# Kernel tuning notes

Hardware: AMD Instinct MI355X
Metric: run time of the kernel (lower is better)

Reference implementation:

```python
import jax, jax.numpy as jnp
import numpy as np

B, S, E, H, L = 64, 256, 640, 512, 2  # batch, seq_len, input_size(=embed+sum_depth), rnn_size, num_layers
ZDIM = L * 2 * 2 * H  # ziphidden output dim = num_layers * num_dirs * (h|c) * H = 4096


def setup_inputs() -> dict:
    key = jax.random.key(0)
    ks = jax.random.split(key, 16)
    s = 0.05  # small init scale (~1/sqrt(H)) to avoid gate saturation
    f32 = jnp.float32
    inp = {
        "input": jax.random.normal(ks[0], (B, S, E), f32),
        "eps": jax.random.normal(ks[1], (B, ZDIM), f32),
        # layer 0 (input E), stacked over 2 directions [fwd, rev]
        "w_ih0": jax.random.normal(ks[2], (2, 4 * H, E), f32) * s,
        "w_hh0": jax.random.normal(ks[3], (2, 4 * H, H), f32) * s,
        "b_ih0": jax.random.normal(ks[4], (2, 4 * H), f32) * s,
        "b_hh0": jax.random.normal(ks[5], (2, 4 * H), f32) * s,
        # layer 1 (input 2H from bidirectional layer-0 output)
        "w_ih1": jax.random.normal(ks[6], (2, 4 * H, 2 * H), f32) * s,
        "w_hh1": jax.random.normal(ks[7], (2, 4 * H, H), f32) * s,
        "b_ih1": jax.random.normal(ks[8], (2, 4 * H), f32) * s,
        "b_hh1": jax.random.normal(ks[9], (2, 4 * H), f32) * s,
        # linear heads (layer_dim*2 -> layer_dim*2)
        "W_mu": jax.random.normal(ks[10], (ZDIM, ZDIM), f32) * 0.02,
        "b_mu": jax.random.normal(ks[11], (ZDIM,), f32) * 0.02,
        "W_var": jax.random.normal(ks[12], (ZDIM, ZDIM), f32) * 0.02,
        "b_var": jax.random.normal(ks[13], (ZDIM,), f32) * 0.02,
    }
    return inp


def _lstm_cell(x, h, c, wih, whh, b):
    # gates order i, f, g, o (PyTorch convention)
    g = x @ wih.T + h @ whh.T + b
    i, f, gg, o = jnp.split(g, 4, axis=-1)
    c2 = jax.nn.sigmoid(f) * c + jax.nn.sigmoid(i) * jnp.tanh(gg)
    h2 = jax.nn.sigmoid(o) * jnp.tanh(c2)
    return h2, c2


def reference(input, eps, w_ih0, w_hh0, b_ih0, b_hh0, w_ih1, w_hh1, b_ih1, b_hh1, W_mu, b_mu, W_var, b_var):
    # Module does input.view(seq_len, batch, embed) (a reshape, not transpose) then
    # steps the LSTM one timestep at a time for seq_len-1 steps. Since each call is
    # a length-1 sequence, both directions see the same single step independently.
    x_seq = input.reshape(S, B, E)[: S - 1]
    W_ih, W_hh = [w_ih0, w_ih1], [w_hh0, w_hh1]
    Bias = [b_ih0 + b_hh0, b_ih1 + b_hh1]

    h0 = jnp.zeros((2 * L, B, H), input.dtype)  # [l0f, l0r, l1f, l1r]
    c0 = jnp.zeros((2 * L, B, H), input.dtype)

    def step(carry, x):
        h, c = carry
        hs, cs = [], []
        inp_l = x
        for l in range(L):
            hf, cf = _lstm_cell(inp_l, h[2 * l], c[2 * l], W_ih[l][0], W_hh[l][0], Bias[l][0])
            hr, cr = _lstm_cell(inp_l, h[2 * l + 1], c[2 * l + 1], W_ih[l][1], W_hh[l][1], Bias[l][1])
            hs += [hf, hr]
            cs += [cf, cr]
            inp_l = jnp.concatenate([hf, hr], axis=-1)  # layer output feeds next layer
        return (jnp.stack(hs), jnp.stack(cs)), None

    (hF, cF), _ = jax.lax.scan(step, (h0, c0), x_seq)

    # ziphidden: cat(h, c, dim=2) -> transpose(0,1) -> view(B, -1)
    z = jnp.concatenate([hF, cF], axis=2)            # [2L, B, 2H]
    z = jnp.transpose(z, (1, 0, 2)).reshape(B, -1)   # [B, ZDIM]

    mu = z @ W_mu.T + b_mu
    logvar = z @ W_var.T + b_var
    # reparameterize (training mode) with externally supplied eps
    return mu + eps * jnp.exp(0.5 * logvar)
```

## Files before the change

kernel.cpp:

```cpp
#include <hip/hip_runtime.h>
#include <hip/hip_bf16.h>
#include <cstddef>
#include <cstdint>

#define B     64
#define S     256
#define E     640
#define H     512
#define TSTEPS (S - 1)
#define ZDIM  4096
#define KT    64
#define HS    (B * H)
#define CELL64 8192
#define NBUF  4

typedef __attribute__((ext_vector_type(8)))  __bf16 bf16x8;
typedef __attribute__((ext_vector_type(16))) float  f32x16;
typedef unsigned long long ull;

__device__ __forceinline__ float sigf(float x) { return 1.0f / (1.0f + __expf(-x)); }
__device__ __forceinline__ float tanhfast(float x) { return 1.0f - 2.0f / (__expf(2.0f * x) + 1.0f); }

__device__ __forceinline__ unsigned short f2bf(float f) {
    union { float f; unsigned u; } x; x.f = f;
    unsigned r = x.u + 0x7fffu + ((x.u >> 16) & 1u);
    return (unsigned short)(r >> 16);
}
__device__ __forceinline__ float bf2f(unsigned short u) {
    union { unsigned u; float f; } x; x.u = ((unsigned)u) << 16;
    return x.f;
}
__device__ __forceinline__ unsigned pk2(float a, float b) {
    return (unsigned)f2bf(a) | ((unsigned)f2bf(b) << 16);
}

#define HSTORE64(p, v) __hip_atomic_store((p), (v), __ATOMIC_RELAXED, __HIP_MEMORY_SCOPE_AGENT)
#define HSTORE32(p, v) __hip_atomic_store((p), (v), __ATOMIC_RELAXED, __HIP_MEMORY_SCOPE_AGENT)

__device__ __forceinline__ uint4 cld16(const void* p) {
    uint4 v;
    asm volatile("global_load_dwordx4 %0, %1, off sc0 sc1"
                 : "=v"(v) : "v"(p) : "memory");
    return v;
}
__device__ __forceinline__ unsigned ldf(const unsigned* p) {
    unsigned v;
    asm volatile("global_load_dword %0, %1, off sc0 sc1"
                 : "=v"(v) : "v"(p) : "memory");
    return v;
}
__device__ __forceinline__ void cwait0() {
    asm volatile("s_waitcnt vmcnt(0)" ::: "memory");
    __builtin_amdgcn_sched_barrier(0);
}
__device__ __forceinline__ bf16x8 u2b(uint4 u) {
    union { uint4 u; bf16x8 b; } x; x.u = u; return x.b;
}


__global__ __launch_bounds__(256) void conv_x_kernel(
    const float* __restrict__ in, unsigned short* __restrict__ out, int n8)
{
    int i = blockIdx.x * 256 + threadIdx.x;
    if (i >= n8) return;
    const float4* p = (const float4*)(in + (size_t)i * 8);
    float4 a = p[0], b = p[1];
    unsigned short* o = out + (size_t)i * 8;
    o[0] = f2bf(a.x); o[1] = f2bf(a.y); o[2] = f2bf(a.z); o[3] = f2bf(a.w);
    o[4] = f2bf(b.x); o[5] = f2bf(b.y); o[6] = f2bf(b.z); o[7] = f2bf(b.w);
}

__global__ __launch_bounds__(256) void repack_w_kernel(
    const float* __restrict__ in, unsigned short* __restrict__ out, int K)
{
    int kc = K / 8;
    int i = blockIdx.x * 256 + threadIdx.x;
    if (i >= 2 * 2048 * kc) return;
    int k8 = i % kc;
    int n  = (i / kc) & 2047;
    int d  = i / (kc * 2048);
    int srow = (n & 3) * 512 + (n >> 2);
    const float* src = in + ((size_t)d * 2048 + srow) * K + (size_t)k8 * 8;
    unsigned short* dst = out + ((size_t)d * 2048 + n) * K + (size_t)k8 * 8;
    #pragma unroll
    for (int q = 0; q < 8; ++q) dst[q] = f2bf(src[q]);
}

__global__ __launch_bounds__(256) void pack_bias_kernel(
    const float* __restrict__ bih, const float* __restrict__ bhh, float* __restrict__ out)
{
    int i = blockIdx.x * 256 + threadIdx.x;
    if (i >= 4096) return;
    int d = i >> 11, n = i & 2047;
    int s = d * 2048 + (n & 3) * 512 + (n >> 2);
    out[i] = bih[s] + bhh[s];
}

__global__ __launch_bounds__(256) void xproj_kernel(
    const unsigned short* __restrict__ xb,
    const unsigned short* __restrict__ w0p,
    unsigned short* __restrict__ xp)
{
    extern __shared__ __align__(16) char lds[];
    const int tid = threadIdx.x;
    const int l   = tid & 63;
    const int w   = tid >> 6;
    const int wm  = w & 1, wn = w >> 1;
    const int d   = blockIdx.x >> 5;
    const int n0  = (blockIdx.x & 31) * 64;

    for (int idx = tid; idx < 64 * 80; idx += 256) {
        int r = idx / 80, k8 = idx % 80;
        bf16x8 v = *(const bf16x8*)(w0p + ((size_t)d*2048 + n0 + r)*640 + (size_t)k8*8);
        int o = k8*16 + r*16; o -= (o >= 1280) ? 1280 : 0;
        *(bf16x8*)(lds + r*1280 + o) = v;
    }
    __syncthreads();

    const int lrow  = wn * 32 + (l & 31);
    const int khalf = l >> 5;
    const char* ldsrow = lds + (size_t)lrow * 1280;
    const int rot = lrow * 16 + khalf * 16;
    const int t0 = blockIdx.y * 64;
    const int t1 = (t0 + 64 < TSTEPS) ? (t0 + 64) : TSTEPS;

    for (int t = t0; t < t1; ++t) {
        f32x16 a0, a1;
#pragma unroll
        for (int r = 0; r < 16; ++r) { a0[r] = 0.f; a1[r] = 0.f; }
        const unsigned short* Ax = xb + ((size_t)t*B + wm*32 + (l & 31))*E + khalf*8;
#pragma unroll 8
        for (int k0 = 0; k0 < E; k0 += 16) {
            bf16x8 a = *(const bf16x8*)(Ax + k0);
            int o = k0*2 + rot; o -= (o >= 1280) ? 1280 : 0;
            bf16x8 b = *(const bf16x8*)(ldsrow + o);
            if ((k0 >> 4) & 1) a1 = __builtin_amdgcn_mfma_f32_32x32x16_bf16(a, b, a1, 0, 0, 0);
            else               a0 = __builtin_amdgcn_mfma_f32_32x32x16_bf16(a, b, a0, 0, 0, 0);
        }
        size_t base = ((((size_t)t*2 + d)*64 + (n0 >> 5) + wn)*2 + wm)*1024 + (size_t)l*16;
        unsigned short* dst = xp + base;
        uint4 o0, o1;
        o0.x = pk2(a0[0]+a1[0],  a0[1]+a1[1]);
        o0.y = pk2(a0[2]+a1[2],  a0[3]+a1[3]);
        o0.z = pk2(a0[4]+a1[4],  a0[5]+a1[5]);
        o0.w = pk2(a0[6]+a1[6],  a0[7]+a1[7]);
        o1.x = pk2(a0[8]+a1[8],  a0[9]+a1[9]);
        o1.y = pk2(a0[10]+a1[10], a0[11]+a1[11]);
        o1.z = pk2(a0[12]+a1[12], a0[13]+a1[13]);
        o1.w = pk2(a0[14]+a1[14], a0[15]+a1[15]);
        *(uint4*)dst       = o0;
        *(uint4*)(dst + 8) = o1;
    }
}

__device__ __forceinline__ void poll_l0(const unsigned* flags, int d,
                                        unsigned traw, unsigned twar, int l)
{
    const unsigned* pd = flags + (size_t)(d*128 + l) * 16;
    const unsigned* p2 = flags + (size_t)(2*128 + l) * 16;
    const unsigned* p3 = flags + (size_t)(3*128 + l) * 16;
    for (;;) {
        unsigned a0 = ldf(pd), a1 = ldf(pd + 64*16);
        unsigned b0 = ldf(p2), b1 = ldf(p2 + 64*16);
        unsigned c0 = ldf(p3), c1 = ldf(p3 + 64*16);
        cwait0();
        unsigned ra = a0 < a1 ? a0 : a1;
        unsigned wb = b0 < b1 ? b0 : b1;
        unsigned wc = c0 < c1 ? c0 : c1;
        unsigned ww = wb < wc ? wb : wc;
        if (__all((int)(ra >= traw && ww >= twar))) break;
        __builtin_amdgcn_s_sleep(1);
    }
}
__device__ __forceinline__ void poll_1c(const unsigned* flags, int cell,
                                        unsigned tgt, int l)
{
    const unsigned* p0 = flags + (size_t)(cell*128 + l) * 16;
    for (;;) {
        unsigned a0 = ldf(p0), a1 = ldf(p0 + 64*16);
        cwait0();
        unsigned v = a0 < a1 ? a0 : a1;
        if (__all((int)(v >= tgt))) break;
        __builtin_amdgcn_s_sleep(1);
    }
}
__device__ __forceinline__ void poll_2c(const unsigned* flags, int ca, int cb,
                                        unsigned tgt, int l)
{
    const unsigned* p0 = flags + (size_t)(ca*128 + l) * 16;
    const unsigned* p1 = flags + (size_t)(cb*128 + l) * 16;
    for (;;) {
        unsigned a0 = ldf(p0), a1 = ldf(p0 + 64*16);
        unsigned b0 = ldf(p1), b1 = ldf(p1 + 64*16);
        cwait0();
        unsigned v = a0 < a1 ? a0 : a1;
        unsigned u = b0 < b1 ? b0 : b1;
        v = v < u ? v : u;
        if (__all((int)(v >= tgt))) break;
        __builtin_amdgcn_s_sleep(1);
    }
}

__device__ __forceinline__ void hcell_c_lds(const void* hp, const char* ldsrow,
    int rotofs, int wrapB, f32x16& a0, f32x16& a1)
{
    uint4 hv[32];
#pragma unroll
    for (int m = 0; m < 32; ++m)
        hv[m] = cld16((const char*)hp + (size_t)m * 1024);
    cwait0();
#pragma unroll
    for (int m = 0; m < 32; ++m) {
        int o = m*32 + rotofs; o -= (o >= wrapB) ? wrapB : 0;
        bf16x8 b = *(const bf16x8*)(ldsrow + o);
        bf16x8 a = u2b(hv[m]);
        if (m & 1) a1 = __builtin_amdgcn_mfma_f32_32x32x16_bf16(a, b, a1, 0, 0, 0);
        else       a0 = __builtin_amdgcn_mfma_f32_32x32x16_bf16(a, b, a0, 0, 0, 0);
    }
}

__device__ __forceinline__ void hcell_c_reg(const void* hp, const bf16x8* wh,
    f32x16& a0, f32x16& a1)
{
    uint4 hv[32];
#pragma unroll
    for (int m = 0; m < 32; ++m)
        hv[m] = cld16((const char*)hp + (size_t)m * 1024);
    cwait0();
#pragma unroll
    for (int m = 0; m < 32; ++m) {
        bf16x8 a = u2b(hv[m]);
        if (m & 1) a1 = __builtin_amdgcn_mfma_f32_32x32x16_bf16(a, wh[m], a1, 0, 0, 0);
        else       a0 = __builtin_amdgcn_mfma_f32_32x32x16_bf16(a, wh[m], a0, 0, 0, 0);
    }
}

template<bool XADD>
__device__ __forceinline__ void act_store(
    const f32x16& a0, const f32x16& a1, bf16x8 xpa, bf16x8 xpb,
    int unitg, int wm, int l, float* creg, float* hreg, ull* hq_cell)
{
    const int g  = l & 3;
    const int hi = l >> 5;
    union { bf16x8 v; unsigned short s[8]; } ua, ub;
    ua.v = xpa; ub.v = xpb;
    float gi[4], gf[4], gg[4], go[4];
#pragma unroll
    for (int r = 0; r < 16; ++r) {
        float v0 = a0[r] + a1[r];
        if (XADD) v0 += bf2f((r < 8) ? ua.s[r] : ub.s[r - 8]);
        float v1 = __shfl_xor(v0, 1);
        float v2 = __shfl_xor(v0, 2);
        float v3 = __shfl_xor(v0, 3);
        float pv[4] = {v0, v1, v2, v3};
        const int rg = r & 3, q = r >> 2;
        if (g == rg) { gi[q] = pv[rg^0]; gf[q] = pv[rg^1]; gg[q] = pv[rg^2]; go[q] = pv[rg^3]; }
    }
    const int ubase = unitg & ~3;
    ull* dst = hq_cell + wm*4096 + (ubase >> 4)*128 + ((ubase >> 3) & 1)*64
                       + ((ubase >> 2) & 1);
#pragma unroll
    for (int q = 0; q < 4; ++q) {
        int rl = g + 8*q + 4*hi;
        float cold = creg[q];
        float cnew = sigf(gf[q]) * cold + sigf(gi[q]) * tanhfast(gg[q]);
        float hnew = sigf(go[q]) * tanhfast(cnew);
        creg[q] = cnew;
        hreg[q] = hnew;
        unsigned m  = f2bf(hnew);
        unsigned o1 = __shfl_xor(m, 4);
        unsigned d0 = (unitg & 1) ? ((m << 16) | o1) : ((o1 << 16) | m);
        unsigned o2 = __shfl_xor(d0, 8);
        ull q64 = (unitg & 2) ? (((ull)d0 << 32) | (ull)o2) : (((ull)o2 << 32) | (ull)d0);
        if ((l & 12) == 0)
            HSTORE64(dst + rl*2, q64);
    }
}

template<int XPRE>
__global__ __launch_bounds__(256, 1) void persist_kernel(
    const unsigned short* __restrict__ xb,
    const unsigned short* __restrict__ w0p,
    const unsigned short* __restrict__ wh0p,
    const unsigned short* __restrict__ w1p,
    const unsigned short* __restrict__ wh1p,
    const float* __restrict__ b0p,
    const float* __restrict__ b1p,
    const unsigned short* __restrict__ xp,
    unsigned short* __restrict__ hbuf,
    float* __restrict__ cbuf,
    unsigned short* __restrict__ hplain,
    unsigned* __restrict__ flags)
{
    extern __shared__ __align__(16) char lds[];
    const int tid = threadIdx.x;
    const int l   = tid & 63;
    const int w   = tid >> 6;
    const int wm  = w & 1, wn = w >> 1;
    const int bid = blockIdx.x;
    const bool isL1 = bid >= 64;
    const int g2 = bid & 63;
    const int d  = g2 >> 5;
    const int n0 = (g2 & 31) * 64;
    const int myslot = g2 & 31;
    const int lrow  = wn * 32 + (l & 31);
    const int khalf = l >> 5;
    const int HHOFF = 64 * 1280;

    if (!isL1) {
        if (!XPRE) {
            for (int idx = tid; idx < 64 * 80; idx += 256) {
                int r = idx / 80, k8 = idx % 80;
                bf16x8 v = *(const bf16x8*)(w0p + ((size_t)d*2048 + n0 + r)*640 + (size_t)k8*8);
                int o = k8*16 + r*16; o -= (o >= 1280) ? 1280 : 0;
                *(bf16x8*)(lds + r*1280 + o) = v;
            }
        }
        const int hb0 = XPRE ? 0 : HHOFF;
        for (int idx = tid; idx < 64 * 64; idx += 256) {
            int r = idx / 64, k8 = idx % 64;
            bf16x8 v = *(const bf16x8*)(wh0p + ((size_t)d*2048 + n0 + r)*512 + (size_t)k8*8);
            int o = k8*16 + r*16; o -= (o >= 1024) ? 1024 : 0;
            *(bf16x8*)(lds + hb0 + r*1024 + o) = v;
        }
    } else {
        for (int idx = tid; idx < 64 * 128; idx += 256) {
            int r = idx / 128, k8 = idx % 128;
            bf16x8 v = *(const bf16x8*)(w1p + ((size_t)d*2048 + n0 + r)*1024 + (size_t)k8*8);
            int o = k8*16 + r*16; o -= (o >= 2048) ? 2048 : 0;
            *(bf16x8*)(lds + r*2048 + o) = v;
        }
    }
    __syncthreads();

    const float bias = (isL1 ? b1p : b0p)[d*2048 + n0 + lrow];
    const char* ldsrow_ih = lds + (size_t)lrow * (isL1 ? 2048 : 1280);
    const char* ldsrow_hh = lds + (XPRE ? 0 : HHOFF) + (size_t)lrow * 1024;
    const int rot = lrow * 16 + khalf * 16;
    const int unitg = ((n0 + lrow) >> 2);
    const int hoff  = wm*4096 + khalf*64 + (l & 31)*2;
    const int arow  = wm * 32 + (l & 31);
    float creg[4] = {0.f, 0.f, 0.f, 0.f};
    float hreg[4] = {0.f, 0.f, 0.f, 0.f};
    const ull* hb = (const ull*)hbuf;
    ull*       hw = (ull*)hbuf;
    const int mycell = isL1 ? (2 + d) : d;
    unsigned* myflag = flags + (size_t)(mycell*128 + myslot*4 + w) * 16;
    bf16x8 zero8 = {};

    bf16x8 wh[32];
    if (isL1) {
        const unsigned short* whl = wh1p + ((size_t)d*2048 + n0 + lrow)*512 + khalf*8;
#pragma unroll
        for (int m = 0; m < 32; ++m) wh[m] = *(const bf16x8*)(whl + m*16);
    }

    for (int k = 0; k <= TSTEPS; ++k) {
        const int rbuf = k % NBUF, wbuf = (k + 1) % NBUF;
        const size_t rb = (size_t)rbuf * 4 * CELL64;
        const size_t wb = (size_t)wbuf * 4 * CELL64;
        if (!isL1) {
            if (k < TSTEPS) {
                f32x16 a0, a1;
#pragma unroll
                for (int r = 0; r < 16; ++r) { a0[r] = bias; a1[r] = 0.f; }
                bf16x8 xpa = zero8, xpb = zero8;
                if (XPRE) {
                    size_t base = ((((size_t)k*2 + d)*64 + (n0 >> 5) + wn)*2 + wm)*1024
                                  + (size_t)l*16;
                    xpa = *(const bf16x8*)(xp + base);
                    xpb = *(const bf16x8*)(xp + base + 8);
                } else {
                    const unsigned short* Ax = xb + (size_t)k*B*E + (size_t)arow*E + khalf*8;
#pragma unroll 8
                    for (int k0 = 0; k0 < E; k0 += 16) {
                        bf16x8 a = *(const bf16x8*)(Ax + k0);
                        int o = k0*2 + rot; o -= (o >= 1280) ? 1280 : 0;
                        bf16x8 b = *(const bf16x8*)(ldsrow_ih + o);
                        if ((k0 >> 4) & 1) a1 = __builtin_amdgcn_mfma_f32_32x32x16_bf16(a, b, a1, 0, 0, 0);
                        else               a0 = __builtin_amdgcn_mfma_f32_32x32x16_bf16(a, b, a0, 0, 0, 0);
                    }
                }
                if (k >= 1)
                    poll_l0(flags, d, (unsigned)k,
                            (k >= 3) ? (unsigned)(k - 3) : 0u, l);
                hcell_c_lds((const char*)(hb + rb + (size_t)d*CELL64 + hoff),
                            ldsrow_hh, rot, 1024, a0, a1);
                act_store<true>(a0, a1, xpa, xpb, unitg, wm, l, creg, hreg,
                                hw + wb + (size_t)d*CELL64);
                asm volatile("s_waitcnt vmcnt(0)" ::: "memory");
                if (l == 0) HSTORE32(myflag, (unsigned)(k + 1));
            }
        } else {
            if (k >= 1) {
                f32x16 a0, a1;
#pragma unroll
                for (int r = 0; r < 16; ++r) { a0[r] = bias; a1[r] = 0.f; }
                if (k >= 2) poll_1c(flags, 2 + d, (unsigned)(k - 1), l);
                hcell_c_reg((const char*)(hb + rb + (size_t)(2+d)*CELL64 + hoff),
                            wh, a0, a1);
                poll_2c(flags, 0, 1, (unsigned)k, l);
                hcell_c_lds((const char*)(hb + rb + (size_t)0*CELL64 + hoff),
                            ldsrow_ih, rot, 2048, a0, a1);
                hcell_c_lds((const char*)(hb + rb + (size_t)1*CELL64 + hoff),
                            ldsrow_ih, rot + 1024, 2048, a0, a1);
                act_store<false>(a0, a1, zero8, zero8, unitg, wm, l, creg, hreg,
                                 hw + wb + (size_t)(2+d)*CELL64);
                asm volatile("s_waitcnt vmcnt(0)" ::: "memory");
                if (l == 0) HSTORE32(myflag, (unsigned)k);
            }
        }
    }

    {
        float*          cc = cbuf   + (size_t)mycell * HS;
        unsigned short* hh = hplain + (size_t)mycell * HS;
        const int g = l & 3, hi = l >> 5;
#pragma unroll
        for (int q = 0; q < 4; ++q) {
            int row = 32*wm + g + 8*q + 4*hi;
            cc[(size_t)row * 512 + unitg] = creg[q];
            hh[(size_t)row * 512 + unitg] = f2bf(hreg[q]);
        }
    }
}

__global__ __launch_bounds__(256) void head_kernel(
    const unsigned short* __restrict__ hplain,
    const float* __restrict__ cbuf,
    const float* __restrict__ eps,
    const float* __restrict__ Wmu,  const float* __restrict__ bmu,
    const float* __restrict__ Wvar, const float* __restrict__ bvar,
    float* __restrict__ out)
{
    const int tid = threadIdx.x;
    const int b   = tid & 63;
    const int i   = blockIdx.x * 4 + (tid >> 6);

    __shared__ float zs[KT][B + 1];

    float amu = 0.f, alv = 0.f;
    const float* wm = Wmu  + (size_t)i * ZDIM;
    const float* wv = Wvar + (size_t)i * ZDIM;

    for (int k0 = 0; k0 < ZDIM; k0 += KT) {
        __syncthreads();
        for (int idx = tid; idx < (B * KT) / 4; idx += 256) {
            int bb  = idx / (KT / 4);
            int kq4 = (idx % (KT / 4)) * 4;
            int zk  = k0 + kq4;
            int cell = zk >> 10;
            int m    = zk & 1023;
            float4 v;
            if (m < H) {
                const unsigned short* hs = hplain + (size_t)cell * HS + (size_t)bb * H + m;
                v.x = bf2f(hs[0]); v.y = bf2f(hs[1]); v.z = bf2f(hs[2]); v.w = bf2f(hs[3]);
            } else {
                v = *(const float4*)(cbuf + (size_t)cell * HS + (size_t)bb * H + (m - H));
            }
            zs[kq4 + 0][bb] = v.x; zs[kq4 + 1][bb] = v.y;
            zs[kq4 + 2][bb] = v.z; zs[kq4 + 3][bb] = v.w;
        }
        __syncthreads();
        #pragma unroll
        for (int kk = 0; kk < KT; kk += 4) {
            float4 a = *(const float4*)(wm + k0 + kk);
            float4 c = *(const float4*)(wv + k0 + kk);
            float z0 = zs[kk + 0][b], z1 = zs[kk + 1][b];
            float z2 = zs[kk + 2][b], z3 = zs[kk + 3][b];
            amu += a.x * z0 + a.y * z1 + a.z * z2 + a.w * z3;
            alv += c.x * z0 + c.y * z1 + c.z * z2 + c.w * z3;
        }
    }
    float mu = amu + bmu[i];
    float lv = alv + bvar[i];
    out[(size_t)b * ZDIM + i] = mu + eps[(size_t)b * ZDIM + i] * __expf(0.5f * lv);
}

extern "C" void kernel_launch(void* const* d_in, const int* in_sizes, int n_in,
                              void* d_out, int out_size, void* d_ws, size_t ws_size,
                              hipStream_t stream) {
    const float* input = (const float*)d_in[0];
    const float* eps   = (const float*)d_in[1];
    const float* w_ih0 = (const float*)d_in[2];
    const float* w_hh0 = (const float*)d_in[3];
    const float* b_ih0 = (const float*)d_in[4];
    const float* b_hh0 = (const float*)d_in[5];
    const float* w_ih1 = (const float*)d_in[6];
    const float* w_hh1 = (const float*)d_in[7];
    const float* b_ih1 = (const float*)d_in[8];
    const float* b_hh1 = (const float*)d_in[9];
    const float* W_mu  = (const float*)d_in[10];
    const float* b_mu  = (const float*)d_in[11];
    const float* W_var = (const float*)d_in[12];
    const float* b_var = (const float*)d_in[13];
    float* out = (float*)d_out;

    uint8_t* base = (uint8_t*)d_ws;
    size_t off = 0;
    auto alloc = [&](size_t bytes) -> void* {
        void* p = base + off;
        off += (bytes + 255) & ~(size_t)255;
        return p;
    };
    unsigned short* xb   = (unsigned short*)alloc((size_t)TSTEPS * B * E * 2);
    unsigned short* w0p  = (unsigned short*)alloc((size_t)2 * 2048 * E * 2);
    unsigned short* wh0p = (unsigned short*)alloc((size_t)2 * 2048 * H * 2);
    unsigned short* w1p  = (unsigned short*)alloc((size_t)2 * 2048 * 1024 * 2);
    unsigned short* wh1p = (unsigned short*)alloc((size_t)2 * 2048 * H * 2);
    float* b0p = (float*)alloc(2 * 2048 * 4);
    float* b1p = (float*)alloc(2 * 2048 * 4);
    unsigned* flags      = (unsigned*)alloc(4 * 128 * 64);
    unsigned short* hbuf = (unsigned short*)alloc((size_t)NBUF * 4 * HS * 2);
    float* cbuf          = (float*)alloc((size_t)4 * HS * 4);
    unsigned short* hplain = (unsigned short*)alloc((size_t)4 * HS * 2);
    unsigned short* xp   = (unsigned short*)alloc((size_t)TSTEPS * 2 * 2048 * B * 2);
    const bool XPRE = (ws_size >= off);

    hipMemsetAsync(flags, 0, 4 * 128 * 64 + (size_t)NBUF * 4 * HS * 2, stream);

    conv_x_kernel<<<(TSTEPS * B * E / 8 + 255) / 256, 256, 0, stream>>>(input, xb, TSTEPS * B * E / 8);
    repack_w_kernel<<<(2 * 2048 * (E / 8) + 255) / 256, 256, 0, stream>>>(w_ih0, w0p, E);
    repack_w_kernel<<<(2 * 2048 * (H / 8) + 255) / 256, 256, 0, stream>>>(w_hh0, wh0p, H);
    repack_w_kernel<<<(2 * 2048 * (1024 / 8) + 255) / 256, 256, 0, stream>>>(w_ih1, w1p, 1024);
    repack_w_kernel<<<(2 * 2048 * (H / 8) + 255) / 256, 256, 0, stream>>>(w_hh1, wh1p, H);
    pack_bias_kernel<<<16, 256, 0, stream>>>(b_ih0, b_hh0, b0p);
    pack_bias_kernel<<<16, 256, 0, stream>>>(b_ih1, b_hh1, b1p);

    const size_t lds_persist = 144 * 1024;
    if (XPRE) {
        const size_t lds_xp = 84 * 1024;
        hipFuncSetAttribute((const void*)xproj_kernel,
                            hipFuncAttributeMaxDynamicSharedMemorySize, (int)lds_xp);
        xproj_kernel<<<dim3(64, 4), 256, lds_xp, stream>>>(xb, w0p, xp);
        hipFuncSetAttribute((const void*)persist_kernel<1>,
                            hipFuncAttributeMaxDynamicSharedMemorySize, (int)lds_persist);
        persist_kernel<1><<<128, 256, lds_persist, stream>>>(
            xb, w0p, wh0p, w1p, wh1p, b0p, b1p, xp, hbuf, cbuf, hplain, flags);
    } else {
        hipFuncSetAttribute((const void*)persist_kernel<0>,
                            hipFuncAttributeMaxDynamicSharedMemorySize, (int)lds_persist);
        persist_kernel<0><<<128, 256, lds_persist, stream>>>(
            xb, w0p, wh0p, w1p, wh1p, b0p, b1p, xp, hbuf, cbuf, hplain, flags);
    }

    head_kernel<<<ZDIM / 4, 256, 0, stream>>>(hplain, cbuf, eps, W_mu, b_mu, W_var, b_var, out);
}
```

Baseline: 3.245 ms.

## Stage shared h tiles through LDS and keep more recurrent weights in registers

In the XPRE path, each block now loads the hidden-state tile once cooperatively across warps (split by wn) into an LDS staging area, instead of every warp loading its own copy from global memory. Layer-0 W_hh moves from LDS into registers. Layer-1 keeps half of W_ih in registers and half in LDS, with the next global load overlapped with the current MFMA consumption. This removes duplicate global loads of h, but adds several __syncthreads per step and raises register pressure from the extra 32-register weight arrays.

```diff
diff --git a/kernel.cpp b/kernel.cpp
--- a/kernel.cpp
+++ b/kernel.cpp
@@ -218,7 +218,6 @@
         else       a0 = __builtin_amdgcn_mfma_f32_32x32x16_bf16(a, b, a0, 0, 0, 0);
     }
 }
-
 __device__ __forceinline__ void hcell_c_reg(const void* hp, const bf16x8* wh,
     f32x16& a0, f32x16& a1)
 {
@@ -233,6 +232,43 @@
         if (m & 1) a1 = __builtin_amdgcn_mfma_f32_32x32x16_bf16(a, wh[m], a1, 0, 0, 0);
         else       a0 = __builtin_amdgcn_mfma_f32_32x32x16_bf16(a, wh[m], a0, 0, 0, 0);
     }
+}
+
+__device__ __forceinline__ void stage_issue(uint4* hv, const char* hpB, int wn) {
+#pragma unroll
+    for (int j = 0; j < 16; ++j)
+        hv[j] = cld16(hpB + (size_t)(wn*16 + j) * 1024);
+}
+__device__ __forceinline__ void stage_write(const uint4* hv, char* stW, int wn) {
+    cwait0();
+#pragma unroll
+    for (int j = 0; j < 16; ++j)
+        *(uint4*)(stW + (size_t)(wn*16 + j) * 1024) = hv[j];
+    __syncthreads();
+}
+__device__ __forceinline__ void consume_reg(const char* stR, const bf16x8* wf,
+                                            f32x16& a0, f32x16& a1)
+{
+#pragma unroll
+    for (int m = 0; m < 32; ++m) {
+        bf16x8 a = *(const bf16x8*)(stR + (size_t)m * 1024);
+        if (m & 1) a1 = __builtin_amdgcn_mfma_f32_32x32x16_bf16(a, wf[m], a1, 0, 0, 0);
+        else       a0 = __builtin_amdgcn_mfma_f32_32x32x16_bf16(a, wf[m], a0, 0, 0, 0);
+    }
+    __syncthreads();
+}
+__device__ __forceinline__ void consume_lds(const char* stR, const char* ldsrow,
+                                            int rot, f32x16& a0, f32x16& a1)
+{
+#pragma unroll
+    for (int m = 0; m < 32; ++m) {
+        bf16x8 a = *(const bf16x8*)(stR + (size_t)m * 1024);
+        int o = (m*32 + rot) & 1023;
+        bf16x8 b = *(const bf16x8*)(ldsrow + o);
+        if (m & 1) a1 = __builtin_amdgcn_mfma_f32_32x32x16_bf16(a, b, a1, 0, 0, 0);
+        else       a0 = __builtin_amdgcn_mfma_f32_32x32x16_bf16(a, b, a0, 0, 0, 0);
+    }
+    __syncthreads();
 }
 
 template<bool XADD>
@@ -307,38 +343,44 @@
     const int khalf = l >> 5;
     const int HHOFF = 64 * 1280;
 
-    if (!isL1) {
-        if (!XPRE) {
+    if (XPRE) {
+        if (isL1) {
+            for (int idx = tid; idx < 64 * 64; idx += 256) {
+                int r = idx >> 6, k8 = idx & 63;
+                bf16x8 v = *(const bf16x8*)(w1p + ((size_t)d*2048 + n0 + r)*1024 + (size_t)k8*8);
+                int o = (k8*16 + r*16) & 1023;
+                *(bf16x8*)(lds + r*1024 + o) = v;
+            }
+        }
+    } else {
+        if (!isL1) {
             for (int idx = tid; idx < 64 * 80; idx += 256) {
                 int r = idx / 80, k8 = idx % 80;
                 bf16x8 v = *(const bf16x8*)(w0p + ((size_t)d*2048 + n0 + r)*640 + (size_t)k8*8);
                 int o = k8*16 + r*16; o -= (o >= 1280) ? 1280 : 0;
                 *(bf16x8*)(lds + r*1280 + o) = v;
             }
-        }
-        const int hb0 = XPRE ? 0 : HHOFF;
-        for (int idx = tid; idx < 64 * 64; idx += 256) {
-            int r = idx / 64, k8 = idx % 64;
-            bf16x8 v = *(const bf16x8*)(wh0p + ((size_t)d*2048 + n0 + r)*512 + (size_t)k8*8);
-            int o = k8*16 + r*16; o -= (o >= 1024) ? 1024 : 0;
-            *(bf16x8*)(lds + hb0 + r*1024 + o) = v;
-        }
-    } else {
-        for (int idx = tid; idx < 64 * 128; idx += 256) {
-            int r = idx / 128, k8 = idx % 128;
-            bf16x8 v = *(const bf16x8*)(w1p + ((size_t)d*2048 + n0 + r)*1024 + (size_t)k8*8);
-            int o = k8*16 + r*16; o -= (o >= 2048) ? 2048 : 0;
-            *(bf16x8*)(lds + r*2048 + o) = v;
+            for (int idx = tid; idx < 64 * 64; idx += 256) {
+                int r = idx / 64, k8 = idx % 64;
+                bf16x8 v = *(const bf16x8*)(wh0p + ((size_t)d*2048 + n0 + r)*512 + (size_t)k8*8);
+                int o = k8*16 + r*16; o -= (o >= 1024) ? 1024 : 0;
+                *(bf16x8*)(lds + HHOFF + r*1024 + o) = v;
+            }
+        } else {
+            for (int idx = tid; idx < 64 * 128; idx += 256) {
+                int r = idx / 128, k8 = idx % 128;
+                bf16x8 v = *(const bf16x8*)(w1p + ((size_t)d*2048 + n0 + r)*1024 + (size_t)k8*8);
+                int o = k8*16 + r*16; o -= (o >= 2048) ? 2048 : 0;
+                *(bf16x8*)(lds + r*2048 + o) = v;
+            }
         }
     }
     __syncthreads();
 
     const float bias = (isL1 ? b1p : b0p)[d*2048 + n0 + lrow];
-    const char* ldsrow_ih = lds + (size_t)lrow * (isL1 ? 2048 : 1280);
-    const char* ldsrow_hh = lds + (XPRE ? 0 : HHOFF) + (size_t)lrow * 1024;
     const int rot = lrow * 16 + khalf * 16;
     const int unitg = ((n0 + lrow) >> 2);
-    const int hoff  = wm*4096 + khalf*64 + (l & 31)*2;
+    const int hoffB = wm*32768 + khalf*512 + (l & 31)*16;
     const int arow  = wm * 32 + (l & 31);
     float creg[4] = {0.f, 0.f, 0.f, 0.f};
     float hreg[4] = {0.f, 0.f, 0.f, 0.f};
@@ -349,11 +391,26 @@
     bf16x8 zero8 = {};
 
     bf16x8 wh[32];
-    if (isL1) {
+    bf16x8 whc1[32];
+    if (XPRE) {
+        const unsigned short* whl = (isL1 ? wh1p : wh0p)
+            + ((size_t)d*2048 + n0 + lrow)*512 + khalf*8;
+#pragma unroll
+        for (int m = 0; m < 32; ++m) wh[m] = *(const bf16x8*)(whl + m*16);
+        if (isL1) {
+            const unsigned short* wcl = w1p + ((size_t)d*2048 + n0 + lrow)*1024 + 512 + khalf*8;
+#pragma unroll
+            for (int m = 0; m < 32; ++m) whc1[m] = *(const bf16x8*)(wcl + m*16);
+        }
+    } else if (isL1) {
         const unsigned short* whl = wh1p + ((size_t)d*2048 + n0 + lrow)*512 + khalf*8;
 #pragma unroll
         for (int m = 0; m < 32; ++m) wh[m] = *(const bf16x8*)(whl + m*16);
     }
+
+    const int STG = isL1 ? 65536 : 0;
+    char* stW = lds + STG + hoffB;
+    const char* ldsihrow = lds + (size_t)lrow * 1024;
 
     for (int k = 0; k <= TSTEPS; ++k) {
         const int rbuf = k % NBUF, wbuf = (k + 1) % NBUF;
@@ -372,6 +429,7 @@
                     xpb = *(const bf16x8*)(xp + base + 8);
                 } else {
                     const unsigned short* Ax = xb + (size_t)k*B*E + (size_t)arow*E + khalf*8;
+                    const char* ldsrow_ih = lds + (size_t)lrow * 1280;
 #pragma unroll 8
                     for (int k0 = 0; k0 < E; k0 += 16) {
                         bf16x8 a = *(const bf16x8*)(Ax + k0);
@@ -384,8 +442,17 @@
                 if (k >= 1)
                     poll_l0(flags, d, (unsigned)k,
                             (k >= 3) ? (unsigned)(k - 3) : 0u, l);
-                hcell_c_lds((const char*)(hb + rb + (size_t)d*CELL64 + hoff),
-                            ldsrow_hh, rot, 1024, a0, a1);
+                const char* hpB = (const char*)(hb + rb + (size_t)d*CELL64) + hoffB;
+                if (XPRE) {
+                    uint4 hv[16];
+                    stage_issue(hv, hpB, wn);
+                    stage_write(hv, stW, wn);
+                    consume_reg(stW, wh, a0, a1);
+                } else {
+                    hcell_c_lds((const char*)(hb + rb + (size_t)d*CELL64)
+                                + (wm*4096 + khalf*64 + (l&31)*2)*8 - hoffB + hoffB,
+                                lds + HHOFF + (size_t)lrow * 1024, rot, 1024, a0, a1);
+                }
                 act_store<true>(a0, a1, xpa, xpb, unitg, wm, l, creg, hreg,
                                 hw + wb + (size_t)d*CELL64);
                 asm volatile("s_waitcnt vmcnt(0)" ::: "memory");
@@ -396,14 +463,29 @@
                 f32x16 a0, a1;
 #pragma unroll
                 for (int r = 0; r < 16; ++r) { a0[r] = bias; a1[r] = 0.f; }
+                const char* hpO = (const char*)(hb + rb + (size_t)(2+d)*CELL64) + hoffB;
+                const char* hp0 = (const char*)(hb + rb + (size_t)0*CELL64) + hoffB;
+                const char* hp1 = (const char*)(hb + rb + (size_t)1*CELL64) + hoffB;
                 if (k >= 2) poll_1c(flags, 2 + d, (unsigned)(k - 1), l);
-                hcell_c_reg((const char*)(hb + rb + (size_t)(2+d)*CELL64 + hoff),
-                            wh, a0, a1);
-                poll_2c(flags, 0, 1, (unsigned)k, l);
-                hcell_c_lds((const char*)(hb + rb + (size_t)0*CELL64 + hoff),
-                            ldsrow_ih, rot, 2048, a0, a1);
-                hcell_c_lds((const char*)(hb + rb + (size_t)1*CELL64 + hoff),
-                            ldsrow_ih, rot + 1024, 2048, a0, a1);
+                if (XPRE) {
+                    uint4 hv[16];
+                    stage_issue(hv, hpO, wn);
+                    stage_write(hv, stW, wn);
+                    poll_2c(flags, 0, 1, (unsigned)k, l);
+                    stage_issue(hv, hp0, wn);
+                    consume_reg(stW, wh, a0, a1);
+                    stage_write(hv, stW, wn);
+                    stage_issue(hv, hp1, wn);
+                    consume_lds(stW, ldsihrow, rot, a0, a1);
+                    stage_write(hv, stW, wn);
+                    consume_reg(stW, whc1, a0, a1);
+                } else {
+                    hcell_c_reg(hpO, wh, a0, a1);
+                    poll_2c(flags, 0, 1, (unsigned)k, l);
+                    const char* ldsrow_ih = lds + (size_t)lrow * 2048;
+                    hcell_c_lds(hp0, ldsrow_ih, rot,        2048, a0, a1);
+                    hcell_c_lds(hp1, ldsrow_ih, rot + 1024, 2048, a0, a1);
+                }
                 act_store<false>(a0, a1, zero8, zero8, unitg, wm, l, creg, hreg,
                                  hw + wb + (size_t)(2+d)*CELL64);
                 asm volatile("s_waitcnt vmcnt(0)" ::: "memory");
```

New measurement: 3.266 ms. About the same (+0.6%).

## Use per-block flags with single-wave polling and pipeline layer-1 hidden loads

Applied to the files above, without the earlier changes.

Replaces the per-wave progress flags with one flag per block, so each poll reads 2 flags per lane instead of 4–6. Only wave 0 polls and then releases the others with a block barrier, and one thread publishes the flag after a barrier. In layer 1 the three hidden-state cell loads are split into 16-wide double-buffered batches using partial vmcnt waits, so MFMAs overlap the next loads. The layer-1 own-cell and cross-layer polls are merged into a single poll before any loads, which drops the earlier overlap of the own-cell matmul with waiting on layer 0 and adds block barriers to the critical path.

```diff
diff --git a/kernel.cpp b/kernel.cpp
--- a/kernel.cpp
+++ b/kernel.cpp
@@ -14,6 +14,8 @@
 #define CELL64 8192
 #define NBUF  4
 
+#define FSLOT(c, s) (((c) << 7) + ((s) << 2))
+
 typedef __attribute__((ext_vector_type(8)))  __bf16 bf16x8;
 typedef __attribute__((ext_vector_type(16))) float  f32x16;
 typedef unsigned long long ull;
@@ -51,6 +53,10 @@
 }
 __device__ __forceinline__ void cwait0() {
     asm volatile("s_waitcnt vmcnt(0)" ::: "memory");
+    __builtin_amdgcn_sched_barrier(0);
+}
+__device__ __forceinline__ void vmw16() {
+    asm volatile("s_waitcnt vmcnt(16)" ::: "memory");
     __builtin_amdgcn_sched_barrier(0);
 }
 __device__ __forceinline__ bf16x8 u2b(uint4 u) {
@@ -156,47 +162,27 @@
 __device__ __forceinline__ void poll_l0(const unsigned* flags, int d,
                                         unsigned traw, unsigned twar, int l)
 {
-    const unsigned* pd = flags + (size_t)(d*128 + l) * 16;
-    const unsigned* p2 = flags + (size_t)(2*128 + l) * 16;
-    const unsigned* p3 = flags + (size_t)(3*128 + l) * 16;
+    const unsigned* pd = flags + FSLOT(d, l & 31);
+    const unsigned* pw = flags + FSLOT((l < 32) ? 2 : 3, l & 31);
     for (;;) {
-        unsigned a0 = ldf(pd), a1 = ldf(pd + 64*16);
-        unsigned b0 = ldf(p2), b1 = ldf(p2 + 64*16);
-        unsigned c0 = ldf(p3), c1 = ldf(p3 + 64*16);
+        unsigned a = ldf(pd);
+        unsigned b = ldf(pw);
         cwait0();
-        unsigned ra = a0 < a1 ? a0 : a1;
-        unsigned wb = b0 < b1 ? b0 : b1;
-        unsigned wc = c0 < c1 ? c0 : c1;
-        unsigned ww = wb < wc ? wb : wc;
-        if (__all((int)(ra >= traw && ww >= twar))) break;
+        if (__all((int)(a >= traw && b >= twar))) break;
         __builtin_amdgcn_s_sleep(1);
     }
 }
-__device__ __forceinline__ void poll_1c(const unsigned* flags, int cell,
-                                        unsigned tgt, int l)
-{
-    const unsigned* p0 = flags + (size_t)(cell*128 + l) * 16;
+__device__ __forceinline__ void poll_l1(const unsigned* flags, int d,
+                                        unsigned k, int l)
+{
+    const unsigned* po = flags + FSLOT(2 + d, l & 31);
+    const unsigned* pc = flags + FSLOT((l < 32) ? 0 : 1, l & 31);
+    const unsigned town = k - 1u;
     for (;;) {
-        unsigned a0 = ldf(p0), a1 = ldf(p0 + 64*16);
+        unsigned a = ldf(po);
+        unsigned b = ldf(pc);
         cwait0();
-        unsigned v = a0 < a1 ? a0 : a1;
-        if (__all((int)(v >= tgt))) break;
-        __builtin_amdgcn_s_sleep(1);
-    }
-}
-__device__ __forceinline__ void poll_2c(const unsigned* flags, int ca, int cb,
-                                        unsigned tgt, int l)
-{
-    const unsigned* p0 = flags + (size_t)(ca*128 + l) * 16;
-    const unsigned* p1 = flags + (size_t)(cb*128 + l) * 16;
-    for (;;) {
-        unsigned a0 = ldf(p0), a1 = ldf(p0 + 64*16);
-        unsigned b0 = ldf(p1), b1 = ldf(p1 + 64*16);
-        cwait0();
-        unsigned v = a0 < a1 ? a0 : a1;
-        unsigned u = b0 < b1 ? b0 : b1;
-        v = v < u ? v : u;
-        if (__all((int)(v >= tgt))) break;
+        if (__all((int)(a >= town && b >= k))) break;
         __builtin_amdgcn_s_sleep(1);
     }
 }
@@ -219,19 +205,33 @@
     }
 }
 
-__device__ __forceinline__ void hcell_c_reg(const void* hp, const bf16x8* wh,
-    f32x16& a0, f32x16& a1)
-{
-    uint4 hv[32];
-#pragma unroll
-    for (int m = 0; m < 32; ++m)
-        hv[m] = cld16((const char*)hp + (size_t)m * 1024);
-    cwait0();
-#pragma unroll
-    for (int m = 0; m < 32; ++m) {
-        bf16x8 a = u2b(hv[m]);
-        if (m & 1) a1 = __builtin_amdgcn_mfma_f32_32x32x16_bf16(a, wh[m], a1, 0, 0, 0);
-        else       a0 = __builtin_amdgcn_mfma_f32_32x32x16_bf16(a, wh[m], a0, 0, 0, 0);
+__device__ __forceinline__ void issue16(uint4* hv, const char* hpB, int mb) {
+#pragma unroll
+    for (int j = 0; j < 16; ++j)
+        hv[j] = cld16(hpB + (size_t)(mb + j) * 1024);
+}
+__device__ __forceinline__ void consume16_reg(const uint4* hv, const bf16x8* wf,
+                                              int mb, f32x16& a0, f32x16& a1)
+{
+#pragma unroll
+    for (int j = 0; j < 16; ++j) {
+        const int m = mb + j;
+        bf16x8 a = u2b(hv[j]);
+        if (m & 1) a1 = __builtin_amdgcn_mfma_f32_32x32x16_bf16(a, wf[m], a1, 0, 0, 0);
+        else       a0 = __builtin_amdgcn_mfma_f32_32x32x16_bf16(a, wf[m], a0, 0, 0, 0);
+    }
+}
+__device__ __forceinline__ void consume16_lds(const uint4* hv, const char* ldsrow,
+                                              int rotofs, int mb, f32x16& a0, f32x16& a1)
+{
+#pragma unroll
+    for (int j = 0; j < 16; ++j) {
+        const int m = mb + j;
+        int o = (m*32 + rotofs) & 2047;
+        bf16x8 b = *(const bf16x8*)(ldsrow + o);
+        bf16x8 a = u2b(hv[j]);
+        if (m & 1) a1 = __builtin_amdgcn_mfma_f32_32x32x16_bf16(a, b, a1, 0, 0, 0);
+        else       a0 = __builtin_amdgcn_mfma_f32_32x32x16_bf16(a, b, a0, 0, 0, 0);
     }
 }
 
@@ -345,7 +345,7 @@
     const ull* hb = (const ull*)hbuf;
     ull*       hw = (ull*)hbuf;
     const int mycell = isL1 ? (2 + d) : d;
-    unsigned* myflag = flags + (size_t)(mycell*128 + myslot*4 + w) * 16;
+    unsigned* myflag = flags + FSLOT(mycell, myslot);
     bf16x8 zero8 = {};
 
     bf16x8 wh[32];
@@ -381,33 +381,48 @@
                         else               a0 = __builtin_amdgcn_mfma_f32_32x32x16_bf16(a, b, a0, 0, 0, 0);
                     }
                 }
-                if (k >= 1)
-                    poll_l0(flags, d, (unsigned)k,
-                            (k >= 3) ? (unsigned)(k - 3) : 0u, l);
+                if (k >= 1) {
+                    if (w == 0)
+                        poll_l0(flags, d, (unsigned)k,
+                                (k >= 3) ? (unsigned)(k - 3) : 0u, l);
+                    __syncthreads();
+                }
                 hcell_c_lds((const char*)(hb + rb + (size_t)d*CELL64 + hoff),
                             ldsrow_hh, rot, 1024, a0, a1);
                 act_store<true>(a0, a1, xpa, xpb, unitg, wm, l, creg, hreg,
                                 hw + wb + (size_t)d*CELL64);
                 asm volatile("s_waitcnt vmcnt(0)" ::: "memory");
-                if (l == 0) HSTORE32(myflag, (unsigned)(k + 1));
+                __syncthreads();
+                if (tid == 0) HSTORE32(myflag, (unsigned)(k + 1));
             }
         } else {
             if (k >= 1) {
                 f32x16 a0, a1;
 #pragma unroll
                 for (int r = 0; r < 16; ++r) { a0[r] = bias; a1[r] = 0.f; }
-                if (k >= 2) poll_1c(flags, 2 + d, (unsigned)(k - 1), l);
-                hcell_c_reg((const char*)(hb + rb + (size_t)(2+d)*CELL64 + hoff),
-                            wh, a0, a1);
-                poll_2c(flags, 0, 1, (unsigned)k, l);
-                hcell_c_lds((const char*)(hb + rb + (size_t)0*CELL64 + hoff),
-                            ldsrow_ih, rot, 2048, a0, a1);
-                hcell_c_lds((const char*)(hb + rb + (size_t)1*CELL64 + hoff),
-                            ldsrow_ih, rot + 1024, 2048, a0, a1);
+                if (w == 0) poll_l1(flags, d, (unsigned)k, l);
+                __syncthreads();
+                const char* hpO = (const char*)(hb + rb + (size_t)(2+d)*CELL64 + hoff);
+                const char* hp0 = (const char*)(hb + rb + (size_t)0*CELL64 + hoff);
+                const char* hp1 = (const char*)(hb + rb + (size_t)1*CELL64 + hoff);
+                uint4 hvA[16], hvB[16];
+                issue16(hvA, hpO, 0);
+                issue16(hvB, hpO, 16);
+                vmw16(); consume16_reg(hvA, wh, 0,  a0, a1);
+                issue16(hvA, hp0, 0);
+                vmw16(); consume16_reg(hvB, wh, 16, a0, a1);
+                issue16(hvB, hp0, 16);
+                vmw16(); consume16_lds(hvA, ldsrow_ih, rot, 0,  a0, a1);
+                issue16(hvA, hp1, 0);
+                vmw16(); consume16_lds(hvB, ldsrow_ih, rot, 16, a0, a1);
+                issue16(hvB, hp1, 16);
+                vmw16(); consume16_lds(hvA, ldsrow_ih, rot + 1024, 0,  a0, a1);
+                cwait0(); consume16_lds(hvB, ldsrow_ih, rot + 1024, 16, a0, a1);
                 act_store<false>(a0, a1, zero8, zero8, unitg, wm, l, creg, hreg,
                                  hw + wb + (size_t)(2+d)*CELL64);
                 asm volatile("s_waitcnt vmcnt(0)" ::: "memory");
-                if (l == 0) HSTORE32(myflag, (unsigned)k);
+                __syncthreads();
+                if (tid == 0) HSTORE32(myflag, (unsigned)k);
             }
         }
     }
@@ -510,14 +525,14 @@
     unsigned short* wh1p = (unsigned short*)alloc((size_t)2 * 2048 * H * 2);
     float* b0p = (float*)alloc(2 * 2048 * 4);
     float* b1p = (float*)alloc(2 * 2048 * 4);
-    unsigned* flags      = (unsigned*)alloc(4 * 128 * 64);
+    unsigned* flags      = (unsigned*)alloc(2048);
     unsigned short* hbuf = (unsigned short*)alloc((size_t)NBUF * 4 * HS * 2);
     float* cbuf          = (float*)alloc((size_t)4 * HS * 4);
     unsigned short* hplain = (unsigned short*)alloc((size_t)4 * HS * 2);
     unsigned short* xp   = (unsigned short*)alloc((size_t)TSTEPS * 2 * 2048 * B * 2);
     const bool XPRE = (ws_size >= off);
 
-    hipMemsetAsync(flags, 0, 4 * 128 * 64 + (size_t)NBUF * 4 * HS * 2, stream);
+    hipMemsetAsync(flags, 0, 2048 + (size_t)NBUF * 4 * HS * 2, stream);
 
     conv_x_kernel<<<(TSTEPS * B * E / 8 + 255) / 256, 256, 0, stream>>>(input, xb, TSTEPS * B * E / 8);
     repack_w_kernel<<<(2 * 2048 * (E / 8) + 255) / 256, 256, 0, stream>>>(w_ih0, w0p, E);
```

New measurement: 2.922 ms. 10.0% less time.
